# Kernel tuning notes

Hardware: AMD Instinct MI355X
Metric: run time of the kernel (lower is better)

The kernel has to match this reference:

```python
import jax, jax.numpy as jnp
import numpy as np

B, T, V, D, H, A = 256, 512, 50000, 256, 256, 128


def setup_inputs() -> dict:
    key = jax.random.key(0)
    ks = jax.random.split(key, 9)
    x = jax.random.randint(ks[0], (B, T), 0, V, dtype=jnp.int32)
    embed_w = jax.random.uniform(ks[1], (V, D), dtype=jnp.float32)          # random_uniform init, non-trainable
    lstm_kernel = jax.random.normal(ks[2], (D + H, 4 * H), dtype=jnp.float32) * 0.05  # BasicLSTMCell kernel [i,j,f,o]
    lstm_bias = jnp.zeros((4 * H,), jnp.float32)
    w_omega = jax.random.normal(ks[3], (H, A), dtype=jnp.float32)
    b_omega = jax.random.normal(ks[4], (A,), dtype=jnp.float32)
    u_omega = jax.random.normal(ks[5], (A,), dtype=jnp.float32)
    w = jax.random.normal(ks[6], (H, 2), dtype=jnp.float32)
    b = jnp.zeros((2,), jnp.float32)
    return {"x": x, "embed_w": embed_w, "lstm_kernel": lstm_kernel,
            "lstm_bias": lstm_bias, "w_omega": w_omega, "b_omega": b_omega,
            "u_omega": u_omega, "w": w, "b": b}


def _lstm_attention_forward(x, embed_w, lstm_kernel, lstm_bias, w_omega, b_omega, u_omega, w, b):
    Bt, Tt = x.shape
    Hh = lstm_bias.shape[0] // 4
    seq_len = jnp.sum(jnp.sign(x), axis=1)                         # [B] like tf.reduce_sum(tf.sign(x))
    e = embed_w[x]                                                  # [B,T,D] embedding lookup
    # dynamic_rnn semantics: outputs zeroed past seq_len, state frozen
    mask = (jnp.arange(Tt)[:, None] < seq_len[None, :]).astype(e.dtype)  # [T,B]
    xs = (jnp.transpose(e, (1, 0, 2)), mask[:, :, None])            # time-major

    def step(carry, inp):
        c, h = carry
        x_t, m = inp                                                # [B,D], [B,1]
        z = jnp.concatenate([x_t, h], axis=-1) @ lstm_kernel + lstm_bias  # [B,4H]
        i, j, f, o = jnp.split(z, 4, axis=-1)
        c_new = c * jax.nn.sigmoid(f + 1.0) + jax.nn.sigmoid(i) * jnp.tanh(j)  # forget_bias=1.0
        h_new = jnp.tanh(c_new) * jax.nn.sigmoid(o)
        c = jnp.where(m > 0, c_new, c)
        h_out = h_new * m
        h = jnp.where(m > 0, h_new, h)
        return (c, h), h_out

    c0 = jnp.zeros((Bt, Hh), e.dtype)
    h0 = jnp.zeros((Bt, Hh), e.dtype)
    _, outs = jax.lax.scan(step, (c0, h0), xs)                      # [T,B,H]
    outs = jnp.transpose(outs, (1, 0, 2))                           # [B,T,H]

    # additive attention pooling
    value = jnp.tanh(jnp.einsum('bth,ha->bta', outs, w_omega) + b_omega)
    vu = jnp.einsum('bta,a->bt', value, u_omega)
    alphas = jax.nn.softmax(vu, axis=-1)                            # [B,T]
    last = jnp.sum(outs * alphas[..., None], axis=1)                # [B,H]

    logits = last @ w + b                                           # [B,2]
    return jax.nn.softmax(logits)


def reference(x, embed_w, lstm_kernel, lstm_bias, w_omega, b_omega, u_omega, w, b):
    return _lstm_attention_forward(x, embed_w, lstm_kernel, lstm_bias,
                                   w_omega, b_omega, u_omega, w, b)
```

## Files before the change

### kernel.cpp

```cpp
#include <hip/hip_runtime.h>
#include <hip/hip_bf16.h>
#include <cstdint>
#include <cstddef>

typedef _Float16 f16;
typedef _Float16 f16x8 __attribute__((ext_vector_type(8)));
typedef _Float16 f16x4 __attribute__((ext_vector_type(4)));
typedef float f32x4 __attribute__((ext_vector_type(4)));
typedef unsigned long long u64;
typedef unsigned int u32;

#define B_   256
#define T_   512
#define V_   50000
#define D_   256
#define H_   256
#define A_   128
#define N4H  1024

__device__ __forceinline__ float sigmoid_f(float x) {
    return __builtin_amdgcn_rcpf(1.f + __expf(-x));
}
__device__ __forceinline__ float tanh_f(float x) {
    float e = __expf(-2.f * fabsf(x));
    float t = 1.f - 2.f * e * __builtin_amdgcn_rcpf(1.f + e);
    return copysignf(t, x);
}

#define MFMA_A(accv, afragv, bfraga)                                         \
    asm volatile("v_mfma_f32_16x16x32_f16 %0, %1, %2, %0"                    \
                 : "+v"(accv) : "v"(afragv), "a"(bfraga))

#define LGKM_BARRIER()                                                       \
    do {                                                                     \
        asm volatile("s_waitcnt lgkmcnt(0)" ::: "memory");                   \
        __builtin_amdgcn_sched_barrier(0);                                   \
        __builtin_amdgcn_s_barrier();                                        \
        __builtin_amdgcn_sched_barrier(0);                                   \
    } while (0)

__global__ __launch_bounds__(256) void k0_convert(
    const float* __restrict__ lstm_kernel, const float* __restrict__ w_omega,
    f16* __restrict__ WxT, f16* __restrict__ WhT, f16* __restrict__ WomT,
    u32* __restrict__ zdone) {
    int blk = blockIdx.x;
    int tau = threadIdx.x;
    if (blk == 0 && tau == 0) *zdone = 0;
    if (blk < N4H) {
        int n = blk;
        WxT[n * 256 + tau] = (f16)lstm_kernel[(size_t)tau * N4H + n];
        WhT[n * 256 + tau] = (f16)lstm_kernel[(size_t)(256 + tau) * N4H + n];
    } else {
        int a = blk - N4H;
        WomT[a * 256 + tau] = (f16)w_omega[(size_t)tau * A_ + a];
    }
}

__global__ __launch_bounds__(256) void k1_seqlen(
    const int* __restrict__ x, int* __restrict__ seqlen) {
    __shared__ int red[256];
    int b = blockIdx.x, tau = threadIdx.x;
    int cnt = (x[b * T_ + tau] != 0) + (x[b * T_ + tau + 256] != 0);
    red[tau] = cnt;
    __syncthreads();
    for (int s = 128; s > 0; s >>= 1) {
        if (tau < s) red[tau] += red[tau + s];
        __syncthreads();
    }
    if (tau == 0) seqlen[b] = red[0];
}

#define SMEM_BYTES 87040

__device__ __forceinline__ void zx_producer(
    const int* __restrict__ x, const float* __restrict__ embed,
    const f16* __restrict__ WxT, const float* __restrict__ bias,
    f16* Zx, int pb, int t0, int Tc, char* smem) {
    f16 (*Ap_s)[264] = (f16(*)[264])smem;
    f16 (*Bp_s)[72]  = (f16(*)[72])(smem + 67584);
    int* tokp_s      = (int*)(smem + 86016);

    int tau  = threadIdx.x;
    int i0   = pb * 128;
    int wave = tau >> 6, lane = tau & 63;
    int q = lane >> 4, c = lane & 15;

    if (tau < 128) {
        int i  = i0 + tau;
        int bb = i / Tc, tr = i - bb * Tc;
        tokp_s[tau] = x[bb * T_ + t0 + tr];
    }
    __syncthreads();

    {
        int r = tau >> 2, quarter = tau & 3;
        const float4* src =
            (const float4*)(embed + (size_t)tokp_s[r] * D_ + quarter * 64);
        f16* dst = &Ap_s[r][quarter * 64];
#pragma unroll
        for (int j = 0; j < 16; j++) {
            float4 v = src[j];
            dst[j * 4 + 0] = (f16)v.x;
            dst[j * 4 + 1] = (f16)v.y;
            dst[j * 4 + 2] = (f16)v.z;
            dst[j * 4 + 3] = (f16)v.w;
        }
    }

    for (int np = 0; np < 8; np++) {
        f32x4 acc[8];
#pragma unroll
        for (int ni = 0; ni < 8; ni++) acc[ni] = (f32x4){0.f, 0.f, 0.f, 0.f};

        for (int kt = 0; kt < 4; kt++) {
            __syncthreads();
            {
                int n = tau >> 2, qt = tau & 3;
                const f16x8* src = (const f16x8*)(WxT +
                    (size_t)(np * 128 + n) * 256 + kt * 64 + qt * 16);
                f16x8* dst = (f16x8*)&Bp_s[n][qt * 16];
                dst[0] = src[0];
                dst[1] = src[1];
            }
            __syncthreads();
#pragma unroll
            for (int s = 0; s < 2; s++) {
                f16x8 afrag =
                    *(const f16x8*)&Ap_s[wave * 16 + c][kt * 64 + s * 32 + q * 8];
#pragma unroll
                for (int ni = 0; ni < 8; ni++) {
                    f16x8 bfrag = *(const f16x8*)&Bp_s[ni * 16 + c][s * 32 + q * 8];
                    acc[ni] = __builtin_amdgcn_mfma_f32_16x16x32_f16(
                        afrag, bfrag, acc[ni], 0, 0, 0);
                }
            }
        }
#pragma unroll
        for (int ni = 0; ni < 8; ni++) {
            int n     = np * 128 + ni * 16 + c;
            int g     = n >> 8, rem = n & 255;
            int halfn = rem >> 7, colu = rem & 127;
            int np2   = halfn * 512 + colu * 4 + g;
            float bv  = bias[n];
#pragma unroll
            for (int r = 0; r < 4; r++) {
                int row = i0 + wave * 16 + q * 4 + r;
                Zx[(size_t)row * N4H + np2] = (f16)(acc[ni][r] + bv);
            }
        }
    }
}

__device__ __forceinline__ void vu_producer(
    const f16* __restrict__ outs, const f16* __restrict__ WomT,
    const float* __restrict__ b_omega, const float* __restrict__ u_omega,
    float* __restrict__ vuout, int b, int t0v, int Tc, char* smem) {
    f16 (*A_s)[264]   = (f16(*)[264])smem;
    f16 (*val_s)[132] = (f16(*)[132])(smem + 33792);
    float* u_s        = (float*)(smem + 50688);

    int tau  = threadIdx.x;
    int wave = tau >> 6, lane = tau & 63;
    int q = lane >> 4, c = lane & 15;

    if (tau < 128) u_s[tau] = u_omega[tau];
    float bom[8];
#pragma unroll
    for (int ni = 0; ni < 8; ni++) bom[ni] = b_omega[ni * 16 + c];

    int nchap = Tc >> 6;
    for (int ch = 0; ch < nchap; ch++) {
        int t0c = t0v + ch * 64;
        __syncthreads();
        if (tau < 256) {
            int r = tau >> 2, seg = tau & 3;
            const f16x8* src =
                (const f16x8*)(outs + ((size_t)b * T_ + t0c + r) * H_ + seg * 64);
            f16x8* dst = (f16x8*)&A_s[r][seg * 64];
#pragma unroll
            for (int j = 0; j < 8; j++) dst[j] = src[j];
        }
        __syncthreads();
        if (tau < 256) {
            f32x4 acc[8];
#pragma unroll
            for (int ni = 0; ni < 8; ni++) acc[ni] = (f32x4){0.f, 0.f, 0.f, 0.f};
#pragma unroll
            for (int kc = 0; kc < 8; kc++) {
                f16x8 afrag = *(const f16x8*)&A_s[wave * 16 + c][kc * 32 + q * 8];
#pragma unroll
                for (int ni = 0; ni < 8; ni++) {
                    f16x8 bfrag = *(const f16x8*)(WomT +
                        (size_t)(ni * 16 + c) * 256 + kc * 32 + q * 8);
                    acc[ni] = __builtin_amdgcn_mfma_f32_16x16x32_f16(
                        afrag, bfrag, acc[ni], 0, 0, 0);
                }
            }
#pragma unroll
            for (int ni = 0; ni < 8; ni++) {
#pragma unroll
                for (int r = 0; r < 4; r++) {
                    val_s[wave * 16 + q * 4 + r][ni * 16 + c] =
                        (f16)tanh_f(acc[ni][r] + bom[ni]);
                }
            }
        }
        __syncthreads();
        if (tau < 64) {
            float s = 0.f;
#pragma unroll 8
            for (int a = 0; a < 128; a++) s += (float)val_s[tau][a] * u_s[a];
            vuout[(size_t)b * T_ + t0c + tau] = s;
        }
    }
}

__global__ __launch_bounds__(512, 2) void k3_lstm(
    const f16* Zx, const f16* __restrict__ WhT,
    const int* __restrict__ seqlen, f16* __restrict__ outs,
    f16* __restrict__ Hstate, float* __restrict__ Cstate,
    u32* __restrict__ Hex, int t0, int Tc, int first, int last,
    const int* __restrict__ x, const float* __restrict__ embed,
    const f16* __restrict__ WxT, const float* __restrict__ bias,
    f16* __restrict__ ZxNext, int t0n, int npz,
    const f16* __restrict__ WomT, const float* __restrict__ b_omega,
    const float* __restrict__ u_omega, float* __restrict__ vuout, int t0v,
    f16* ZxCurW, int nz0, u32* __restrict__ zdone) {
    __shared__ __align__(16) char smem[SMEM_BYTES];

    if (blockIdx.x >= 32) {
        int pid = blockIdx.x - 32;
        if (pid < nz0) {
            zx_producer(x, embed, WxT, bias, ZxCurW, pid, t0, Tc, smem);
            __syncthreads();
            if (threadIdx.x == 0)
                __hip_atomic_fetch_add(zdone, 1u, __ATOMIC_RELEASE,
                                       __HIP_MEMORY_SCOPE_AGENT);
        } else if (pid - nz0 < npz) {
            zx_producer(x, embed, WxT, bias, ZxNext, pid - nz0, t0n, Tc, smem);
        } else {
            vu_producer(outs, WomT, b_omega, u_omega, vuout, pid - nz0 - npz,
                        t0v, Tc, smem);
        }
        return;
    }

    f16 (*Zx_s)[16][520] = (f16(*)[16][520])smem;
    f16 (*h_s)[16][264]  = (f16(*)[16][264])(smem + 33280);

    int tau  = threadIdx.x;
    int w    = tau >> 6, lane = tau & 63;
    int q = lane >> 4, c = lane & 15;
    int wgid = blockIdx.x;
    int pair = wgid >> 1, half = wgid & 1;
    int b0 = pair * 16;
    int u0 = half * 128, pu0 = (half ^ 1) * 128;
    int u  = u0 + w * 16 + c;
    int col = w * 16 + c;

    u32* hexw_my = Hex + (size_t)wgid * 2 * 2048;
    u32* hexw_pr = Hex + (size_t)(wgid ^ 1) * 2 * 2048;

    f32x4 wha[4][8];
#pragma unroll
    for (int g = 0; g < 4; g++)
#pragma unroll
        for (int s = 0; s < 8; s++) {
            int kc = (s < 4) ? (half * 4 + s) : ((half ^ 1) * 4 + (s - 4));
            f16x8 f = *(const f16x8*)(WhT +
                (size_t)(g * 256 + u0 + w * 16 + c) * 256 + kc * 32 + q * 8);
            f32x4 t = __builtin_bit_cast(f32x4, f);
            asm volatile("" : "=a"(wha[g][s]) : "0"(t));
        }

    int kOwn = half * 128 + q * 8;
    int kPar = (half ^ 1) * 128 + q * 8;

    int p0 = t0 & 1;
    if (first) {
        for (int idx = tau; idx < 2 * 16 * 264; idx += 512)
            ((f16*)h_s)[idx] = (f16)0.f;
    } else {
        for (int idx = tau; idx < 16 * 256; idx += 512) {
            int r = idx >> 8, k = idx & 255;
            h_s[p0][r][k] = Hstate[(b0 + r) * H_ + k];
        }
    }

    float cst[4];
    f16   hprev[4];
    int   sl[4];
#pragma unroll
    for (int r = 0; r < 4; r++) {
        int row = q * 4 + r;
        cst[r]   = first ? 0.f : Cstate[(b0 + row) * H_ + u];
        hprev[r] = first ? (f16)0.f : Hstate[(b0 + row) * H_ + u];
        sl[r]    = seqlen[b0 + row];
    }

    if (first) {
        if (tau == 0) {
            while (__hip_atomic_load(zdone, __ATOMIC_ACQUIRE,
                                     __HIP_MEMORY_SCOPE_AGENT) < (u32)nz0) {}
        }
        __syncthreads();
    }

    int r_st = tau >> 5;
    int cc   = (tau & 31) * 16;
    const f16* zxrow = Zx + ((size_t)(b0 + r_st) * Tc) * N4H + half * 512 + cc;

    {
        const f16x8* src = (const f16x8*)zxrow;
        f16x8* dst = (f16x8*)&Zx_s[p0][r_st][cc];
        dst[0] = src[0];
        dst[1] = src[1];
    }
    int rr = tau >> 5;
    int uu = (tau & 31) * 4;

    __syncthreads();

    f32x4 accO[4];
#pragma unroll
    for (int g = 0; g < 4; g++) accO[g] = (f32x4){0.f, 0.f, 0.f, 0.f};
#pragma unroll
    for (int kk = 0; kk < 4; kk++) {
        f16x8 afrag = *(const f16x8*)&h_s[p0][c][kOwn + kk * 32];
#pragma unroll
        for (int g = 0; g < 4; g++) MFMA_A(accO[g], afrag, wha[g][kk]);
    }

    u64 vp0 = 0, vp1 = 0;

    for (int tt = 0; tt < Tc; tt++) {
        int t   = t0 + tt;
        int cur = t & 1, nxt = cur ^ 1;

        int tn = (tt + 1 < Tc) ? tt + 1 : tt;
        const f16x8* psrc = (const f16x8*)(zxrow + (size_t)tn * N4H);
        f16x8 z0 = psrc[0];
        f16x8 z1 = psrc[1];

        if (tt > 0) {
            u32 tagp = (u32)(t & 0xffff);
            const u64* pp = (const u64*)&hexw_pr[cur * 2048 + rr * 128 + uu];
            while (((u32)(vp0 >> 16) & 0xffffu) != tagp ||
                   ((u32)(vp0 >> 48)) != tagp ||
                   ((u32)(vp1 >> 16) & 0xffffu) != tagp ||
                   ((u32)(vp1 >> 48)) != tagp) {
                vp0 = __hip_atomic_load(pp + 0, __ATOMIC_RELAXED,
                                        __HIP_MEMORY_SCOPE_AGENT);
                vp1 = __hip_atomic_load(pp + 1, __ATOMIC_RELAXED,
                                        __HIP_MEMORY_SCOPE_AGENT);
            }
            u64 hw = (u64)(vp0 & 0xffff) | (((vp0 >> 32) & 0xffff) << 16) |
                     ((vp1 & 0xffff) << 32) | (((vp1 >> 32) & 0xffff) << 48);
            *(u64*)&h_s[cur][rr][pu0 + uu] = hw;
        }
        LGKM_BARRIER();

#pragma unroll
        for (int kk = 0; kk < 4; kk++) {
            f16x8 afrag = *(const f16x8*)&h_s[cur][c][kPar + kk * 32];
#pragma unroll
            for (int g = 0; g < 4; g++) MFMA_A(accO[g], afrag, wha[g][4 + kk]);
        }

        u32 tag = (u32)((t + 1) & 0xffff);
        f16 ovals[4];
#pragma unroll
        for (int r = 0; r < 4; r++) {
            int row = q * 4 + r;
            f16x4 zv = *(const f16x4*)&Zx_s[cur][row][col * 4];
            float zi = accO[0][r] + (float)zv[0];
            float zj = accO[1][r] + (float)zv[1];
            float zf = accO[2][r] + (float)zv[2];
            float zo = accO[3][r] + (float)zv[3];
            float ig = sigmoid_f(zi);
            float jg = tanh_f(zj);
            float fg = sigmoid_f(zf + 1.f);
            float og = sigmoid_f(zo);
            float cn = cst[r] * fg + ig * jg;
            float hn = tanh_f(cn) * og;
            bool  m  = (t < sl[r]);
            cst[r]   = m ? cn : cst[r];
            f16 hkeep = m ? (f16)hn : hprev[r];
            hprev[r]  = hkeep;
            h_s[nxt][row][u] = hkeep;
            u32 word = (tag << 16) |
                       (u32)(unsigned short)__builtin_bit_cast(short, hkeep);
            __hip_atomic_store(&hexw_my[nxt * 2048 + row * 128 + col], word,
                               __ATOMIC_RELAXED, __HIP_MEMORY_SCOPE_AGENT);
            ovals[r] = m ? (f16)hn : (f16)0.f;
        }

        {
            f16x8* dst = (f16x8*)&Zx_s[nxt][r_st][cc];
            dst[0] = z0;
            dst[1] = z1;
        }

#pragma unroll
        for (int r = 0; r < 4; r++)
            outs[((size_t)(b0 + q * 4 + r) * T_ + t) * H_ + u] = ovals[r];

        {
            const u64* pp2 = (const u64*)&hexw_pr[nxt * 2048 + rr * 128 + uu];
            vp0 = __hip_atomic_load(pp2 + 0, __ATOMIC_RELAXED,
                                    __HIP_MEMORY_SCOPE_AGENT);
            vp1 = __hip_atomic_load(pp2 + 1, __ATOMIC_RELAXED,
                                    __HIP_MEMORY_SCOPE_AGENT);
        }

        LGKM_BARRIER();

#pragma unroll
        for (int g = 0; g < 4; g++) accO[g] = (f32x4){0.f, 0.f, 0.f, 0.f};
#pragma unroll
        for (int kk = 0; kk < 4; kk++) {
            f16x8 afrag = *(const f16x8*)&h_s[nxt][c][kOwn + kk * 32];
#pragma unroll
            for (int g = 0; g < 4; g++) MFMA_A(accO[g], afrag, wha[g][kk]);
        }
    }

    if (!last) {
        int parity = (t0 + Tc) & 1;
        for (int idx = tau; idx < 16 * 128; idx += 512) {
            int r = idx >> 7, k = u0 + (idx & 127);
            Hstate[(b0 + r) * H_ + k] = h_s[parity][r][k];
        }
#pragma unroll
        for (int r = 0; r < 4; r++)
            Cstate[(b0 + q * 4 + r) * H_ + u] = cst[r];
    }
}

__global__ __launch_bounds__(512) void k4_attn(
    const f16* __restrict__ outs, const f16* __restrict__ WomT,
    const float* __restrict__ b_omega, const float* __restrict__ u_omega,
    const float* __restrict__ w, const float* __restrict__ bfin,
    const float* __restrict__ vuin, int tstart, float* __restrict__ out) {
    __shared__ __align__(16) f16 A_s[64][264];
    __shared__ __align__(16) f16 val_s[64][132];
    __shared__ float u_s[128];
    __shared__ float vu_s[512];
    __shared__ float red0[512], red1[512];

    int b = blockIdx.x, tau = threadIdx.x;
    int wave = tau >> 6, lane = tau & 63;
    int q = lane >> 4, c = lane & 15;

    if (tau < 128) u_s[tau] = u_omega[tau];
    float bom[8];
#pragma unroll
    for (int ni = 0; ni < 8; ni++) bom[ni] = b_omega[ni * 16 + c];

    for (int t = tau; t < tstart; t += 512) vu_s[t] = vuin[(size_t)b * T_ + t];

    for (int ch = tstart >> 6; ch < 8; ch++) {
        int t0c = ch * 64;
        __syncthreads();
        if (tau < 256) {
            int r = tau >> 2, seg = tau & 3;
            const f16x8* src =
                (const f16x8*)(outs + ((size_t)b * T_ + t0c + r) * H_ + seg * 64);
            f16x8* dst = (f16x8*)&A_s[r][seg * 64];
#pragma unroll
            for (int j = 0; j < 8; j++) dst[j] = src[j];
        }
        __syncthreads();
        if (tau < 256) {
            f32x4 acc[8];
#pragma unroll
            for (int ni = 0; ni < 8; ni++) acc[ni] = (f32x4){0.f, 0.f, 0.f, 0.f};
#pragma unroll
            for (int kc = 0; kc < 8; kc++) {
                f16x8 afrag = *(const f16x8*)&A_s[wave * 16 + c][kc * 32 + q * 8];
#pragma unroll
                for (int ni = 0; ni < 8; ni++) {
                    f16x8 bfrag = *(const f16x8*)(WomT +
                        (size_t)(ni * 16 + c) * 256 + kc * 32 + q * 8);
                    acc[ni] = __builtin_amdgcn_mfma_f32_16x16x32_f16(
                        afrag, bfrag, acc[ni], 0, 0, 0);
                }
            }
#pragma unroll
            for (int ni = 0; ni < 8; ni++) {
#pragma unroll
                for (int r = 0; r < 4; r++) {
                    val_s[wave * 16 + q * 4 + r][ni * 16 + c] =
                        (f16)tanh_f(acc[ni][r] + bom[ni]);
                }
            }
        }
        __syncthreads();
        if (tau < 64) {
            float s = 0.f;
#pragma unroll 8
            for (int a = 0; a < 128; a++) s += (float)val_s[tau][a] * u_s[a];
            vu_s[t0c + tau] = s;
        }
    }
    __syncthreads();

    red0[tau] = vu_s[tau];
    __syncthreads();
    for (int s = 256; s > 0; s >>= 1) {
        if (tau < s) red0[tau] = fmaxf(red0[tau], red0[tau + s]);
        __syncthreads();
    }
    float mx = red0[0];
    __syncthreads();
    float e = __expf(vu_s[tau] - mx);
    red0[tau] = e;
    __syncthreads();
    for (int s = 256; s > 0; s >>= 1) {
        if (tau < s) red0[tau] += red0[tau + s];
        __syncthreads();
    }
    float inv = 1.f / red0[0];
    __syncthreads();
    vu_s[tau] = e * inv;
    __syncthreads();

    int h = tau & 255, tg = tau >> 8;
    float lastv = 0.f;
    {
        const f16* orow = outs + ((size_t)b * T_ + tg * 256) * H_ + h;
        const float* al = &vu_s[tg * 256];
#pragma unroll 4
        for (int t = 0; t < 256; t++)
            lastv += al[t] * (float)orow[(size_t)t * H_];
    }
    red0[tau] = lastv;
    __syncthreads();
    float lsum = (tau < 256) ? red0[tau] + red0[tau + 256] : 0.f;
    __syncthreads();

    red0[tau] = (tau < 256) ? lsum * w[h * 2 + 0] : 0.f;
    red1[tau] = (tau < 256) ? lsum * w[h * 2 + 1] : 0.f;
    __syncthreads();
    for (int s = 256; s > 0; s >>= 1) {
        if (tau < s) {
            red0[tau] += red0[tau + s];
            red1[tau] += red1[tau + s];
        }
        __syncthreads();
    }
    if (tau == 0) {
        float l0 = red0[0] + bfin[0], l1 = red1[0] + bfin[1];
        float mm = fmaxf(l0, l1);
        float a0 = __expf(l0 - mm), a1 = __expf(l1 - mm);
        float den = a0 + a1;
        out[b * 2 + 0] = a0 / den;
        out[b * 2 + 1] = a1 / den;
    }
}

extern "C" void kernel_launch(void* const* d_in, const int* in_sizes, int n_in,
                              void* d_out, int out_size, void* d_ws,
                              size_t ws_size, hipStream_t stream) {
    const int*   x           = (const int*)d_in[0];
    const float* embed       = (const float*)d_in[1];
    const float* lstm_kernel = (const float*)d_in[2];
    const float* lstm_bias   = (const float*)d_in[3];
    const float* w_omega     = (const float*)d_in[4];
    const float* b_omega     = (const float*)d_in[5];
    const float* u_omega     = (const float*)d_in[6];
    const float* w           = (const float*)d_in[7];
    const float* bfin        = (const float*)d_in[8];
    float*       out         = (float*)d_out;

    char* ws = (char*)d_ws;
    f16*   WxT    = (f16*)(ws + 0);
    f16*   WhT    = (f16*)(ws + 524288);
    f16*   WomT   = (f16*)(ws + 1048576);
    int*   seqlen = (int*)(ws + 1114112);
    f16*   Hstate = (f16*)(ws + 1115136);
    float* Cstate = (float*)(ws + 1246208);
    u32*   Hex    = (u32*)(ws + 1508352);
    u32*   zdone  = (u32*)(ws + 2032640);
    float* vu     = (float*)(ws + 2033664);
    f16*   outs   = (f16*)(ws + 2557952);

    const size_t fixed = 2557952ull + 67108864ull;
    int nch = 1;
    while (nch < 16 && fixed + 2ull * (268435456ull / (size_t)nch) > ws_size)
        nch <<= 1;
    int Tc = T_ / nch;
    size_t chunkB = 268435456ull / (size_t)nch;
    f16* ZxA = (f16*)(ws + fixed);
    f16* ZxB = (f16*)(ws + fixed + chunkB);

    int vuEnable = (Tc % 64 == 0) && (nch >= 2);
    int tstart   = vuEnable ? (nch - 1) * Tc : 0;
    int nz0all   = (B_ * Tc) / 128;

    k0_convert<<<1152, 256, 0, stream>>>(lstm_kernel, w_omega, WxT, WhT, WomT,
                                         zdone);
    k1_seqlen<<<256, 256, 0, stream>>>(x, seqlen);
    for (int chk = 0; chk < nch; chk++) {
        int  t0  = chk * Tc;
        f16* zc  = (chk & 1) ? ZxB : ZxA;
        f16* zn  = (chk & 1) ? ZxA : ZxB;
        int  nzp = (chk == 0) ? nz0all : 0;
        int  npz = (chk + 1 < nch) ? (B_ * Tc) / 128 : 0;
        int  nv  = (vuEnable && chk >= 1) ? B_ : 0;
        int  t0n = (chk + 1) * Tc;
        int  t0v = (chk - 1) * Tc;
        k3_lstm<<<32 + nzp + npz + nv, 512, 0, stream>>>(
            zc, WhT, seqlen, outs, Hstate, Cstate, Hex, t0, Tc,
            chk == 0 ? 1 : 0, chk == nch - 1 ? 1 : 0,
            x, embed, WxT, lstm_bias, zn, t0n, npz,
            WomT, b_omega, u_omega, vu, t0v,
            zc, nzp, zdone);
    }
    k4_attn<<<256, 512, 0, stream>>>(outs, WomT, b_omega, u_omega, w, bfin,
                                     vu, tstart, out);
}
```

Before: 1.503 ms.

## Split first-chunk Zx projection into its own kernel and merge seqlen into convert

The first chunk's input projection no longer runs inside the LSTM launch with an atomic counter and spin-wait. It now runs as a separate kernel before the recurrent loop, so the recurrent blocks no longer contend with producer blocks or poll a global flag. The seqlen reduction is folded into the weight-conversion kernel to save one launch. The cost is that the first chunk's projection is fully serialized before the LSTM starts, losing the overlap the in-kernel producer scheme allowed.

```diff
diff --git a/kernel.cpp b/kernel.cpp
--- a/kernel.cpp
+++ b/kernel.cpp
@@ -42,32 +42,28 @@
 __global__ __launch_bounds__(256) void k0_convert(
     const float* __restrict__ lstm_kernel, const float* __restrict__ w_omega,
     f16* __restrict__ WxT, f16* __restrict__ WhT, f16* __restrict__ WomT,
-    u32* __restrict__ zdone) {
+    const int* __restrict__ x, int* __restrict__ seqlen) {
+    __shared__ int red[256];
     int blk = blockIdx.x;
     int tau = threadIdx.x;
-    if (blk == 0 && tau == 0) *zdone = 0;
     if (blk < N4H) {
         int n = blk;
         WxT[n * 256 + tau] = (f16)lstm_kernel[(size_t)tau * N4H + n];
         WhT[n * 256 + tau] = (f16)lstm_kernel[(size_t)(256 + tau) * N4H + n];
-    } else {
+    } else if (blk < N4H + A_) {
         int a = blk - N4H;
         WomT[a * 256 + tau] = (f16)w_omega[(size_t)tau * A_ + a];
-    }
-}
-
-__global__ __launch_bounds__(256) void k1_seqlen(
-    const int* __restrict__ x, int* __restrict__ seqlen) {
-    __shared__ int red[256];
-    int b = blockIdx.x, tau = threadIdx.x;
-    int cnt = (x[b * T_ + tau] != 0) + (x[b * T_ + tau + 256] != 0);
-    red[tau] = cnt;
-    __syncthreads();
-    for (int s = 128; s > 0; s >>= 1) {
-        if (tau < s) red[tau] += red[tau + s];
-        __syncthreads();
-    }
-    if (tau == 0) seqlen[b] = red[0];
+    } else {
+        int b = blk - (N4H + A_);
+        int cnt = (x[b * T_ + tau] != 0) + (x[b * T_ + tau + 256] != 0);
+        red[tau] = cnt;
+        __syncthreads();
+        for (int s = 128; s > 0; s >>= 1) {
+            if (tau < s) red[tau] += red[tau + s];
+            __syncthreads();
+        }
+        if (tau == 0) seqlen[b] = red[0];
+    }
 }
 
 #define SMEM_BYTES 87040
@@ -75,7 +71,7 @@
 __device__ __forceinline__ void zx_producer(
     const int* __restrict__ x, const float* __restrict__ embed,
     const f16* __restrict__ WxT, const float* __restrict__ bias,
-    f16* Zx, int pb, int t0, int Tc, char* smem) {
+    f16* __restrict__ Zx, int pb, int t0, int Tc, char* smem) {
     f16 (*Ap_s)[264] = (f16(*)[264])smem;
     f16 (*Bp_s)[72]  = (f16(*)[72])(smem + 67584);
     int* tokp_s      = (int*)(smem + 86016);
@@ -151,6 +147,14 @@
     }
 }
 
+__global__ __launch_bounds__(512) void k2b_zx(
+    const int* __restrict__ x, const float* __restrict__ embed,
+    const f16* __restrict__ WxT, const float* __restrict__ bias,
+    f16* __restrict__ Zx, int t0, int Tc) {
+    __shared__ __align__(16) char smem[SMEM_BYTES];
+    zx_producer(x, embed, WxT, bias, Zx, blockIdx.x, t0, Tc, smem);
+}
+
 __device__ __forceinline__ void vu_producer(
     const f16* __restrict__ outs, const f16* __restrict__ WomT,
     const float* __restrict__ b_omega, const float* __restrict__ u_omega,
@@ -216,7 +220,7 @@
 }
 
 __global__ __launch_bounds__(512, 2) void k3_lstm(
-    const f16* Zx, const f16* __restrict__ WhT,
+    const f16* __restrict__ Zx, const f16* __restrict__ WhT,
     const int* __restrict__ seqlen, f16* __restrict__ outs,
     f16* __restrict__ Hstate, float* __restrict__ Cstate,
     u32* __restrict__ Hex, int t0, int Tc, int first, int last,
@@ -224,24 +228,16 @@
     const f16* __restrict__ WxT, const float* __restrict__ bias,
     f16* __restrict__ ZxNext, int t0n, int npz,
     const f16* __restrict__ WomT, const float* __restrict__ b_omega,
-    const float* __restrict__ u_omega, float* __restrict__ vuout, int t0v,
-    f16* ZxCurW, int nz0, u32* __restrict__ zdone) {
+    const float* __restrict__ u_omega, float* __restrict__ vuout, int t0v) {
     __shared__ __align__(16) char smem[SMEM_BYTES];
 
     if (blockIdx.x >= 32) {
         int pid = blockIdx.x - 32;
-        if (pid < nz0) {
-            zx_producer(x, embed, WxT, bias, ZxCurW, pid, t0, Tc, smem);
-            __syncthreads();
-            if (threadIdx.x == 0)
-                __hip_atomic_fetch_add(zdone, 1u, __ATOMIC_RELEASE,
-                                       __HIP_MEMORY_SCOPE_AGENT);
-        } else if (pid - nz0 < npz) {
-            zx_producer(x, embed, WxT, bias, ZxNext, pid - nz0, t0n, Tc, smem);
-        } else {
-            vu_producer(outs, WomT, b_omega, u_omega, vuout, pid - nz0 - npz,
-                        t0v, Tc, smem);
-        }
+        if (pid < npz)
+            zx_producer(x, embed, WxT, bias, ZxNext, pid, t0n, Tc, smem);
+        else
+            vu_producer(outs, WomT, b_omega, u_omega, vuout, pid - npz, t0v,
+                        Tc, smem);
         return;
     }
 
@@ -296,14 +292,6 @@
         cst[r]   = first ? 0.f : Cstate[(b0 + row) * H_ + u];
         hprev[r] = first ? (f16)0.f : Hstate[(b0 + row) * H_ + u];
         sl[r]    = seqlen[b0 + row];
-    }
-
-    if (first) {
-        if (tau == 0) {
-            while (__hip_atomic_load(zdone, __ATOMIC_ACQUIRE,
-                                     __HIP_MEMORY_SCOPE_AGENT) < (u32)nz0) {}
-        }
-        __syncthreads();
     }
 
     int r_st = tau >> 5;
@@ -581,11 +569,10 @@
     f16*   Hstate = (f16*)(ws + 1115136);
     float* Cstate = (float*)(ws + 1246208);
     u32*   Hex    = (u32*)(ws + 1508352);
-    u32*   zdone  = (u32*)(ws + 2032640);
-    float* vu     = (float*)(ws + 2033664);
-    f16*   outs   = (f16*)(ws + 2557952);
-
-    const size_t fixed = 2557952ull + 67108864ull;
+    float* vu     = (float*)(ws + 2032640);
+    f16*   outs   = (f16*)(ws + 2556928);
+
+    const size_t fixed = 2556928ull + 67108864ull;
     int nch = 1;
     while (nch < 16 && fixed + 2ull * (268435456ull / (size_t)nch) > ws_size)
         nch <<= 1;
@@ -596,26 +583,24 @@
 
     int vuEnable = (Tc % 64 == 0) && (nch >= 2);
     int tstart   = vuEnable ? (nch - 1) * Tc : 0;
-    int nz0all   = (B_ * Tc) / 128;
-
-    k0_convert<<<1152, 256, 0, stream>>>(lstm_kernel, w_omega, WxT, WhT, WomT,
-                                         zdone);
-    k1_seqlen<<<256, 256, 0, stream>>>(x, seqlen);
+
+    k0_convert<<<N4H + A_ + B_, 256, 0, stream>>>(lstm_kernel, w_omega, WxT,
+                                                  WhT, WomT, x, seqlen);
+    k2b_zx<<<(B_ * Tc) / 128, 512, 0, stream>>>(x, embed, WxT, lstm_bias, ZxA,
+                                                0, Tc);
     for (int chk = 0; chk < nch; chk++) {
         int  t0  = chk * Tc;
         f16* zc  = (chk & 1) ? ZxB : ZxA;
         f16* zn  = (chk & 1) ? ZxA : ZxB;
-        int  nzp = (chk == 0) ? nz0all : 0;
         int  npz = (chk + 1 < nch) ? (B_ * Tc) / 128 : 0;
         int  nv  = (vuEnable && chk >= 1) ? B_ : 0;
         int  t0n = (chk + 1) * Tc;
         int  t0v = (chk - 1) * Tc;
-        k3_lstm<<<32 + nzp + npz + nv, 512, 0, stream>>>(
+        k3_lstm<<<32 + npz + nv, 512, 0, stream>>>(
             zc, WhT, seqlen, outs, Hstate, Cstate, Hex, t0, Tc,
             chk == 0 ? 1 : 0, chk == nch - 1 ? 1 : 0,
             x, embed, WxT, lstm_bias, zn, t0n, npz,
-            WomT, b_omega, u_omega, vu, t0v,
-            zc, nzp, zdone);
+            WomT, b_omega, u_omega, vu, t0v);
     }
     k4_attn<<<256, 512, 0, stream>>>(outs, WomT, b_omega, u_omega, w, bfin,
                                      vu, tstart, out);
```

Result: faster. 1.436 ms, median of 3 (-4.4%).
